# Kernel tuning notes

Hardware: AMD Instinct MI355X
Metric: run time of the kernel (lower is better)

The kernel has to match this reference:

```python
import jax, jax.numpy as jnp
import numpy as np

SINUSOIDAL_EMBEDDING_BASE = 10000.0
WEIGHT_INIT_SCALE = 0.02
B = 524288
X_DIM = 128
T_EMB_DIM = 32
HIDDEN = 64
INPUT_DIM = 1 + X_DIM + T_EMB_DIM  # 161


def timestep_embedding(t, dim):
    # t: [B] int or float -> [B, dim] sinusoidal embedding
    half = dim // 2
    freqs = jnp.exp(-jnp.log(jnp.float32(SINUSOIDAL_EMBEDDING_BASE)) * jnp.arange(half, dtype=jnp.float32) / half)
    args = t[:, None].astype(jnp.float32) * freqs[None, :]
    emb = jnp.concatenate([jnp.sin(args), jnp.cos(args)], axis=1)
    if dim % 2 == 1:
        emb = jnp.concatenate([emb, jnp.zeros((t.shape[0], 1), dtype=emb.dtype)], axis=1)
    return emb


def setup_inputs() -> dict:
    key = jax.random.key(0)
    k1, k2, k3, k4, k5 = jax.random.split(key, 5)
    y_t = jax.random.normal(k1, (B, 1), dtype=jnp.float32)
    t = jax.random.randint(k2, (B,), 0, 1000, dtype=jnp.int32)
    x = jax.random.normal(k3, (B, X_DIM), dtype=jnp.float32)
    fc1_weight = jax.random.normal(k4, (HIDDEN, INPUT_DIM), dtype=jnp.float32) * WEIGHT_INIT_SCALE
    fc1_bias = jnp.zeros((HIDDEN,), dtype=jnp.float32)
    fc2_weight = jax.random.normal(k5, (1, HIDDEN), dtype=jnp.float32) * WEIGHT_INIT_SCALE
    fc2_bias = jnp.zeros((1,), dtype=jnp.float32)
    return {"y_t": y_t, "t": t, "x": x,
            "fc1_weight": fc1_weight, "fc1_bias": fc1_bias,
            "fc2_weight": fc2_weight, "fc2_bias": fc2_bias}


def reference(y_t, t, x, fc1_weight, fc1_bias, fc2_weight, fc2_bias):
    te = timestep_embedding(t, T_EMB_DIM)              # [B, t_emb_dim]
    inp = jnp.concatenate([y_t, x, te], axis=1)        # [B, input_dim]
    # The original's per-unit loop (sum(inp * W[i]) + b[i]) is exactly a matmul.
    h = jax.nn.relu(inp @ fc1_weight.T + fc1_bias)     # [B, hidden]
    out = h @ fc2_weight.T + fc2_bias                  # [B, 1]
    return out
```

## Files before the change

kernel.cpp:

```cpp
#include <hip/hip_runtime.h>
#include <hip/hip_bf16.h>


typedef __bf16 bf16x8 __attribute__((ext_vector_type(8)));
typedef float  f32x4  __attribute__((ext_vector_type(4)));

#define NROWS   524288
#define KSTEPS  6
#define NTILES  4

static __device__ inline unsigned short f2bf(float x) {
    union { float f; unsigned u; } v; v.f = x;
    unsigned r = v.u + 0x7FFFu + ((v.u >> 16) & 1u);
    return (unsigned short)(r >> 16);
}

static __device__ inline bf16x8 cvt8(float4 a, float4 b) {
    uint4 r;
    r.x = (unsigned)f2bf(a.x) | ((unsigned)f2bf(a.y) << 16);
    r.y = (unsigned)f2bf(a.z) | ((unsigned)f2bf(a.w) << 16);
    r.z = (unsigned)f2bf(b.x) | ((unsigned)f2bf(b.y) << 16);
    r.w = (unsigned)f2bf(b.z) | ((unsigned)f2bf(b.w) << 16);
    return __builtin_bit_cast(bf16x8, r);
}

__global__ void setup_te_table(unsigned short* __restrict__ tab) {
    int tid = blockIdx.x * blockDim.x + threadIdx.x;
    if (tid >= 16000) return;
    int t = tid >> 4;
    int j = tid & 15;
    float e    = (-9.2103403719761836f * (float)j) * 0.0625f;
    float freq = expf(e);
    float a    = (float)t * freq;
    tab[t * 32 + j]      = f2bf(sinf(a));
    tab[t * 32 + 16 + j] = f2bf(cosf(a));
}

__global__ void setup_w_frags(const float* __restrict__ w1, const float* __restrict__ b1,
                              unsigned short* __restrict__ wf) {
    int tid = blockIdx.x * blockDim.x + threadIdx.x;
    int l  = tid & 63;
    int fs = tid >> 6;
    int n  = fs / 6;
    int s  = fs % 6;
    int col = 16 * n + (l & 15);
    int g   = l >> 4;
    unsigned short vals[8] __attribute__((aligned(16)));
    #pragma unroll
    for (int j = 0; j < 8; ++j) {
        int k = 32 * s + 8 * g + j;
        float v;
        if      (k < 160)  v = w1[col * 161 + k + 1];
        else if (k == 160) v = w1[col * 161 + 0];
        else if (k == 161) v = b1[col];
        else               v = 0.0f;
        vals[j] = f2bf(v);
    }
    ((uint4*)wf)[tid] = *(const uint4*)vals;
}

__global__ __launch_bounds__(256) void mlp_kernel(
    const float* __restrict__ y_t, const int* __restrict__ t, const float* __restrict__ x,
    const float* __restrict__ w2, const float* __restrict__ b2p,
    const unsigned short* __restrict__ wfrag, const unsigned short* __restrict__ tetab,
    float* __restrict__ out)
{
    const int tid = threadIdx.x;
    const int l   = tid & 63;
    const int wv  = tid >> 6;
    const int r   = l & 15;
    const int g   = l >> 4;
    const long long blockRow0 = (long long)blockIdx.x * 128;

    float w2f[4];
    #pragma unroll
    for (int n = 0; n < NTILES; ++n) w2f[n] = w2[16 * n + r];
    const float b2 = b2p[0];

    const bf16x8* __restrict__ wfv = (const bf16x8*)wfrag;

    #pragma unroll
    for (int mtI = 0; mtI < 2; ++mtI) {
        const int mt = wv * 2 + mtI;
        const long long arow = blockRow0 + mt * 16 + r;

        bf16x8 af[KSTEPS];
        const float4* __restrict__ xrow = (const float4*)(x + arow * 128);
        #pragma unroll
        for (int s = 0; s < 4; ++s) {
            float4 a = xrow[8 * s + 2 * g];
            float4 b = xrow[8 * s + 2 * g + 1];
            af[s] = cvt8(a, b);
        }
        {
            int tval = t[arow];
            tval = tval < 0 ? 0 : (tval > 999 ? 999 : tval);
            af[4] = *(const bf16x8*)(tetab + tval * 32 + 8 * g);
        }
        {
            uint4 u = make_uint4(0u, 0u, 0u, 0u);
            if (g == 0) u.x = (unsigned)f2bf(y_t[arow]) | (0x3F80u << 16);
            af[5] = __builtin_bit_cast(bf16x8, u);
        }

        f32x4 acc[NTILES];
        #pragma unroll
        for (int n = 0; n < NTILES; ++n) acc[n] = (f32x4){0.f, 0.f, 0.f, 0.f};
        #pragma unroll
        for (int n = 0; n < NTILES; ++n)
            #pragma unroll
            for (int s = 0; s < KSTEPS; ++s)
                acc[n] = __builtin_amdgcn_mfma_f32_16x16x32_bf16(
                    af[s], wfv[(n * 6 + s) * 64 + l], acc[n], 0, 0, 0);

        float4 p;
        float* pp = &p.x;
        #pragma unroll
        for (int v = 0; v < 4; ++v) {
            float pv = 0.f;
            #pragma unroll
            for (int n = 0; n < NTILES; ++n) pv += w2f[n] * fmaxf(acc[n][v], 0.f);
            pv += __shfl_xor(pv, 1);
            pv += __shfl_xor(pv, 2);
            pv += __shfl_xor(pv, 4);
            pv += __shfl_xor(pv, 8);
            pp[v] = pv + b2;
        }
        if (r == 0) {
            *(float4*)(out + blockRow0 + mt * 16 + g * 4) = p;
        }
    }
}

extern "C" void kernel_launch(void* const* d_in, const int* in_sizes, int n_in,
                              void* d_out, int out_size, void* d_ws, size_t ws_size,
                              hipStream_t stream) {
    const float* y_t = (const float*)d_in[0];
    const int*   t   = (const int*)  d_in[1];
    const float* x   = (const float*)d_in[2];
    const float* w1  = (const float*)d_in[3];
    const float* b1  = (const float*)d_in[4];
    const float* w2  = (const float*)d_in[5];
    const float* b2  = (const float*)d_in[6];

    unsigned short* wfrag = (unsigned short*)d_ws;
    unsigned short* tetab = wfrag + 12288;

    setup_w_frags <<<6,  256, 0, stream>>>(w1, b1, wfrag);
    setup_te_table<<<63, 256, 0, stream>>>(tetab);
    mlp_kernel<<<NROWS / 128, 256, 0, stream>>>(y_t, t, x, w2, b2, wfrag, tetab, (float*)d_out);
}
```

Measured before the change: 377.9 us.

## Stage x rows through LDS via direct global-to-LDS loads with swizzle

Each wave now handles a single 16-row tile. It loads that tile's x rows into LDS using coalesced global_load_lds 16-byte transfers with an XOR swizzle, then reads the MFMA A-fragments from LDS. The previous strided per-row float4 global reads are removed. The two setup kernels are merged into one launch, the grid is doubled with 64 rows per block, and launch_bounds requests 4 blocks per CU. The costs are 32KB of LDS per block, which limits occupancy, and an exposed full vmcnt wait with no overlap of the load.

```diff
diff --git a/kernel.cpp b/kernel.cpp
--- a/kernel.cpp
+++ b/kernel.cpp
@@ -24,111 +24,130 @@
     return __builtin_bit_cast(bf16x8, r);
 }
 
-__global__ void setup_te_table(unsigned short* __restrict__ tab) {
-    int tid = blockIdx.x * blockDim.x + threadIdx.x;
-    if (tid >= 16000) return;
-    int t = tid >> 4;
-    int j = tid & 15;
-    float e    = (-9.2103403719761836f * (float)j) * 0.0625f;
-    float freq = expf(e);
-    float a    = (float)t * freq;
-    tab[t * 32 + j]      = f2bf(sinf(a));
-    tab[t * 32 + 16 + j] = f2bf(cosf(a));
+static __device__ inline void gload_lds16(const void* g, void* l) {
+    __builtin_amdgcn_global_load_lds(
+        (const __attribute__((address_space(1))) unsigned int*)g,
+        (__attribute__((address_space(3))) unsigned int*)l, 16, 0, 0);
 }
 
-__global__ void setup_w_frags(const float* __restrict__ w1, const float* __restrict__ b1,
-                              unsigned short* __restrict__ wf) {
+__global__ void setup_tables(const float* __restrict__ w1, const float* __restrict__ b1,
+                             unsigned short* __restrict__ wf, unsigned short* __restrict__ tab) {
     int tid = blockIdx.x * blockDim.x + threadIdx.x;
-    int l  = tid & 63;
-    int fs = tid >> 6;
-    int n  = fs / 6;
-    int s  = fs % 6;
-    int col = 16 * n + (l & 15);
-    int g   = l >> 4;
-    unsigned short vals[8] __attribute__((aligned(16)));
-    #pragma unroll
-    for (int j = 0; j < 8; ++j) {
-        int k = 32 * s + 8 * g + j;
-        float v;
-        if      (k < 160)  v = w1[col * 161 + k + 1];
-        else if (k == 160) v = w1[col * 161 + 0];
-        else if (k == 161) v = b1[col];
-        else               v = 0.0f;
-        vals[j] = f2bf(v);
+    if (tid < 1536) {
+        int l  = tid & 63;
+        int fs = tid >> 6;
+        int n  = fs / 6;
+        int s  = fs % 6;
+        int col = 16 * n + (l & 15);
+        int g   = l >> 4;
+        unsigned short vals[8] __attribute__((aligned(16)));
+        #pragma unroll
+        for (int j = 0; j < 8; ++j) {
+            int k = 32 * s + 8 * g + j;
+            float v;
+            if      (k < 160)  v = w1[col * 161 + k + 1];
+            else if (k == 160) v = w1[col * 161 + 0];
+            else if (k == 161) v = b1[col];
+            else               v = 0.0f;
+            vals[j] = f2bf(v);
+        }
+        ((uint4*)wf)[tid] = *(const uint4*)vals;
     }
-    ((uint4*)wf)[tid] = *(const uint4*)vals;
+    if (tid < 16000) {
+        int t = tid >> 4;
+        int j = tid & 15;
+        float freq = expf((-9.2103403719761836f * (float)j) * 0.0625f);
+        float a    = (float)t * freq;
+        tab[t * 32 + j]      = f2bf(sinf(a));
+        tab[t * 32 + 16 + j] = f2bf(cosf(a));
+    }
 }
 
-__global__ __launch_bounds__(256) void mlp_kernel(
+__global__ __launch_bounds__(256, 4) void mlp_kernel(
     const float* __restrict__ y_t, const int* __restrict__ t, const float* __restrict__ x,
     const float* __restrict__ w2, const float* __restrict__ b2p,
     const unsigned short* __restrict__ wfrag, const unsigned short* __restrict__ tetab,
     float* __restrict__ out)
 {
+    __shared__ __align__(16) float ldsx[64 * 128];
     const int tid = threadIdx.x;
     const int l   = tid & 63;
     const int wv  = tid >> 6;
     const int r   = l & 15;
     const int g   = l >> 4;
-    const long long blockRow0 = (long long)blockIdx.x * 128;
+    const long long trow0 = (long long)blockIdx.x * 64 + wv * 16;
+    const long long arow  = trow0 + r;
+
+    int   tval = t[arow];
+    float yv   = y_t[arow];
 
     float w2f[4];
     #pragma unroll
     for (int n = 0; n < NTILES; ++n) w2f[n] = w2[16 * n + r];
     const float b2 = b2p[0];
 
-    const bf16x8* __restrict__ wfv = (const bf16x8*)wfrag;
+    {
+        const int rr = l >> 5;
+        const int c  = l & 31;
+        #pragma unroll
+        for (int i = 0; i < 8; ++i) {
+            const int rowrel = 2 * i + rr;
+            const int csrc   = c ^ (rowrel & 7);
+            const float* src = x + (trow0 + rowrel) * 128 + csrc * 4;
+            gload_lds16(src, (void*)(ldsx + wv * 2048 + i * 256));
+        }
+    }
+    asm volatile("s_waitcnt vmcnt(0)" ::: "memory");
 
-    #pragma unroll
-    for (int mtI = 0; mtI < 2; ++mtI) {
-        const int mt = wv * 2 + mtI;
-        const long long arow = blockRow0 + mt * 16 + r;
-
-        bf16x8 af[KSTEPS];
-        const float4* __restrict__ xrow = (const float4*)(x + arow * 128);
+    bf16x8 af[KSTEPS];
+    {
+        const float4* lx = (const float4*)ldsx;
+        const int base = wv * 512 + r * 32;
+        const int sw   = r & 7;
         #pragma unroll
         for (int s = 0; s < 4; ++s) {
-            float4 a = xrow[8 * s + 2 * g];
-            float4 b = xrow[8 * s + 2 * g + 1];
+            int c0 = 8 * s + 2 * g;
+            float4 a = lx[base + ((c0    ) ^ sw)];
+            float4 b = lx[base + ((c0 + 1) ^ sw)];
             af[s] = cvt8(a, b);
         }
-        {
-            int tval = t[arow];
-            tval = tval < 0 ? 0 : (tval > 999 ? 999 : tval);
-            af[4] = *(const bf16x8*)(tetab + tval * 32 + 8 * g);
-        }
-        {
-            uint4 u = make_uint4(0u, 0u, 0u, 0u);
-            if (g == 0) u.x = (unsigned)f2bf(y_t[arow]) | (0x3F80u << 16);
-            af[5] = __builtin_bit_cast(bf16x8, u);
-        }
+    }
+    {
+        tval = tval < 0 ? 0 : (tval > 999 ? 999 : tval);
+        af[4] = *(const bf16x8*)(tetab + tval * 32 + 8 * g);
+    }
+    {
+        uint4 u = make_uint4(0u, 0u, 0u, 0u);
+        if (g == 0) u.x = (unsigned)f2bf(yv) | (0x3F80u << 16);
+        af[5] = __builtin_bit_cast(bf16x8, u);
+    }
 
-        f32x4 acc[NTILES];
+    const bf16x8* __restrict__ wfv = (const bf16x8*)wfrag;
+    f32x4 acc[NTILES];
+    #pragma unroll
+    for (int n = 0; n < NTILES; ++n) acc[n] = (f32x4){0.f, 0.f, 0.f, 0.f};
+    #pragma unroll
+    for (int n = 0; n < NTILES; ++n)
         #pragma unroll
-        for (int n = 0; n < NTILES; ++n) acc[n] = (f32x4){0.f, 0.f, 0.f, 0.f};
+        for (int s = 0; s < KSTEPS; ++s)
+            acc[n] = __builtin_amdgcn_mfma_f32_16x16x32_bf16(
+                af[s], wfv[(n * 6 + s) * 64 + l], acc[n], 0, 0, 0);
+
+    float4 p;
+    float* pp = &p.x;
+    #pragma unroll
+    for (int v = 0; v < 4; ++v) {
+        float pv = 0.f;
         #pragma unroll
-        for (int n = 0; n < NTILES; ++n)
-            #pragma unroll
-            for (int s = 0; s < KSTEPS; ++s)
-                acc[n] = __builtin_amdgcn_mfma_f32_16x16x32_bf16(
-                    af[s], wfv[(n * 6 + s) * 64 + l], acc[n], 0, 0, 0);
-
-        float4 p;
-        float* pp = &p.x;
-        #pragma unroll
-        for (int v = 0; v < 4; ++v) {
-            float pv = 0.f;
-            #pragma unroll
-            for (int n = 0; n < NTILES; ++n) pv += w2f[n] * fmaxf(acc[n][v], 0.f);
-            pv += __shfl_xor(pv, 1);
-            pv += __shfl_xor(pv, 2);
-            pv += __shfl_xor(pv, 4);
-            pv += __shfl_xor(pv, 8);
-            pp[v] = pv + b2;
-        }
-        if (r == 0) {
-            *(float4*)(out + blockRow0 + mt * 16 + g * 4) = p;
-        }
+        for (int n = 0; n < NTILES; ++n) pv += w2f[n] * fmaxf(acc[n][v], 0.f);
+        pv += __shfl_xor(pv, 1);
+        pv += __shfl_xor(pv, 2);
+        pv += __shfl_xor(pv, 4);
+        pv += __shfl_xor(pv, 8);
+        pp[v] = pv + b2;
+    }
+    if (r == 0) {
+        *(float4*)(out + trow0 + 4 * g) = p;
     }
 }
 
@@ -146,7 +165,6 @@
     unsigned short* wfrag = (unsigned short*)d_ws;
     unsigned short* tetab = wfrag + 12288;
 
-    setup_w_frags <<<6,  256, 0, stream>>>(w1, b1, wfrag);
-    setup_te_table<<<63, 256, 0, stream>>>(tetab);
-    mlp_kernel<<<NROWS / 128, 256, 0, stream>>>(y_t, t, x, w2, b2, wfrag, tetab, (float*)d_out);
+    setup_tables<<<64, 256, 0, stream>>>(w1, b1, wfrag, tetab);
+    mlp_kernel<<<NROWS / 64, 256, 0, stream>>>(y_t, t, x, w2, b2, wfrag, tetab, (float*)d_out);
 }
```

After: 385.8 us. +2.1%, slower.
